# Kernel tuning notes

Hardware: AMD Instinct MI355X
Metric: run time of the kernel (lower is better)

## Reference

```python
import jax, jax.numpy as jnp
import numpy as np

B, T, D, F, E = 2, 2048, 1024, 4096, 8
TOP_K = 2


def setup_inputs() -> dict:
    key = jax.random.key(0)
    k0, k1, k2, k3 = jax.random.split(key, 4)
    x = jax.random.normal(k0, (B, T, D), dtype=jnp.float32)
    Wr = jax.random.normal(k1, (D, E), dtype=jnp.float32) * 0.02   # router (no bias)
    W1 = jax.random.normal(k2, (E, D, F), dtype=jnp.float32) * 0.02
    b1 = jnp.zeros((E, F), dtype=jnp.float32)
    W2 = jax.random.normal(k3, (E, F, D), dtype=jnp.float32) * 0.02
    b2 = jnp.zeros((E, D), dtype=jnp.float32)
    return {"x": x, "Wr": Wr, "W1": W1, "b1": b1, "W2": W2, "b2": b2}


def reference(x, Wr, W1, b1, W2, b2):
    # Router: softmax over experts, top-k select, renormalize selected probs.
    logits = jnp.einsum('btd,de->bte', x, Wr)                      # [B,T,E]
    probs = jax.nn.softmax(logits, axis=-1)
    top_v, top_i = jax.lax.top_k(probs, TOP_K)                     # [B,T,K]
    top_v = top_v / jnp.sum(top_v, axis=-1, keepdims=True)
    # Combine weights: scatter renormalized top-k probs back to expert slots.
    combine = jnp.sum(jax.nn.one_hot(top_i, E, dtype=x.dtype) * top_v[..., None], axis=-2)  # [B,T,E]
    # Expert FFNs (Linear -> exact GELU -> Linear); dropout inactive at eval.
    h = jax.nn.gelu(jnp.einsum('btd,edf->ebtf', x, W1) + b1[:, None, None, :],
                    approximate=False)                              # [E,B,T,F]
    y = jnp.einsum('ebtf,efd->ebtd', h, W2) + b2[:, None, None, :]  # [E,B,T,D]
    # Weighted sum over selected experts (combine is zero for unselected).
    out = jnp.einsum('ebtd,bte->btd', y, combine)
    return out
```

## Files before the change

### kernel.cpp

```cpp
#include <hip/hip_runtime.h>
#include <hip/hip_bf16.h>
#include <math.h>

#define B_  2
#define T_  2048
#define D_  1024
#define F_  4096
#define E_  8
#define NTOK 4096
#define TOPK 2
#define NROW 8192

typedef unsigned short bf16_t;
typedef float f32x4 __attribute__((ext_vector_type(4)));
typedef int   i32x4 __attribute__((ext_vector_type(4)));

#define OFF_CNT   0
#define OFF_BASE  32
#define OFF_TIDX  64
#define OFF_TW    32832
#define OFF_LIST  65600
#define OFF_WGT   196672
#define OFF_H_OLD 327744
#define WS_OLD    (OFF_H_OLD + (size_t)NROW * F_ * 2)
#define OFF_SLOT  327744
#define OFF_XB    (1u << 20)
#define OFF_W1T   (OFF_XB  + (size_t)NTOK * D_ * 2)
#define OFF_W2T   (OFF_W1T + (size_t)E_ * F_ * D_ * 2)
#define OFF_HN    (OFF_W2T + (size_t)E_ * D_ * F_ * 2)
#define OFF_Y     (OFF_HN  + (size_t)NROW * F_ * 2)
#define WS_MFMA   (OFF_Y + (size_t)NROW * D_ * 4)
#define WS_MFMA2  (OFF_Y + 2 * (size_t)NROW * D_ * 4)

__device__ __forceinline__ float gelu_exact(float v) {
    return 0.5f * v * (1.0f + erff(v * 0.70710678118654752440f));
}

__device__ __forceinline__ unsigned short f2bf_rne(float f) {
    union { float f; unsigned int u; } v; v.f = f;
    unsigned int r = (v.u + 0x7fffu + ((v.u >> 16) & 1u)) >> 16;
    return (unsigned short)r;
}

__device__ __forceinline__ float bf2f(unsigned int u) {
    union { unsigned int i; float f; } v; v.i = u << 16; return v.f;
}

__device__ __forceinline__ void gld16(const void* g, void* l) {
    __builtin_amdgcn_global_load_lds(
        (const __attribute__((address_space(1))) unsigned int*)g,
        (__attribute__((address_space(3))) unsigned int*)l, 16, 0, 0);
}

__device__ __forceinline__ void mfma16(const i32x4& a, const i32x4& b, f32x4& c) {
    asm("v_mfma_f32_16x16x32_bf16 %0, %1, %2, %0" : "+v"(c) : "v"(a), "v"(b));
}

__global__ __launch_bounds__(64) void router_kernel(
    const float* __restrict__ x, const float* __restrict__ Wr,
    int* __restrict__ top_idx, float* __restrict__ top_w,
    int* __restrict__ cnt, int* __restrict__ list, float* __restrict__ wgt,
    int* __restrict__ slot, int mode)
{
    const int n = blockIdx.x;
    const int lane = threadIdx.x;
    const float* xr = x + (size_t)n * D_;

    float acc[E_];
#pragma unroll
    for (int e = 0; e < E_; ++e) acc[e] = 0.f;

    for (int d = lane; d < D_; d += 64) {
        const float xv = xr[d];
#pragma unroll
        for (int e = 0; e < E_; ++e)
            acc[e] += xv * Wr[d * E_ + e];
    }
#pragma unroll
    for (int e = 0; e < E_; ++e) {
        float v = acc[e];
#pragma unroll
        for (int off = 32; off > 0; off >>= 1)
            v += __shfl_down(v, off, 64);
        acc[e] = v;
    }
    if (lane == 0) {
        float m = acc[0];
#pragma unroll
        for (int e = 1; e < E_; ++e) m = fmaxf(m, acc[e]);
        float p[E_];
#pragma unroll
        for (int e = 0; e < E_; ++e) p[e] = __expf(acc[e] - m);
        int i0 = 0; float v0 = p[0];
#pragma unroll
        for (int e = 1; e < E_; ++e) if (p[e] > v0) { v0 = p[e]; i0 = e; }
        int i1 = (i0 == 0) ? 1 : 0; float v1 = p[i1];
#pragma unroll
        for (int e = 0; e < E_; ++e) {
            if (e == i0) continue;
            if (p[e] > v1) { v1 = p[e]; i1 = e; }
        }
        const float inv = 1.f / (v0 + v1);
        const float w0 = v0 * inv, w1 = v1 * inv;
        top_idx[n * TOPK + 0] = i0;
        top_idx[n * TOPK + 1] = i1;
        top_w[n * TOPK + 0] = w0;
        top_w[n * TOPK + 1] = w1;
        if (mode & 1) {
            int p0 = atomicAdd(&cnt[i0], 1);
            list[i0 * NTOK + p0] = n;  wgt[i0 * NTOK + p0] = w0;
            int p1 = atomicAdd(&cnt[i1], 1);
            list[i1 * NTOK + p1] = n;  wgt[i1 * NTOK + p1] = w1;
            if (mode & 2) {
                slot[n * TOPK + 0] = (i0 << 16) | p0;
                slot[n * TOPK + 1] = (i1 << 16) | p1;
            }
        }
    }
}

__global__ void prefix_kernel(const int* __restrict__ cnt, int* __restrict__ base)
{
    if (threadIdx.x == 0 && blockIdx.x == 0) {
        int s = 0;
#pragma unroll
        for (int e = 0; e < E_; ++e) { base[e] = s; s += cnt[e]; }
    }
}

__global__ __launch_bounds__(256) void convert_x_kernel(
    const float* __restrict__ x, bf16_t* __restrict__ xb)
{
    const int i = blockIdx.x * 256 + threadIdx.x;
    const float4 v = ((const float4*)x)[i];
    uint2 o;
    o.x = (unsigned int)f2bf_rne(v.x) | ((unsigned int)f2bf_rne(v.y) << 16);
    o.y = (unsigned int)f2bf_rne(v.z) | ((unsigned int)f2bf_rne(v.w) << 16);
    ((uint2*)xb)[i] = o;
}

__global__ __launch_bounds__(256) void transpose_kernel(
    const float* __restrict__ src, bf16_t* __restrict__ dst, int R, int C)
{
    __shared__ float tile[64][65];
    const int z  = blockIdx.z;
    const int r0 = blockIdx.y * 64;
    const int c0 = blockIdx.x * 64;
    const float* s = src + (size_t)z * R * C;
    bf16_t*      d = dst + (size_t)z * R * C;
    const int tx = threadIdx.x & 63;
    const int ty = threadIdx.x >> 6;
#pragma unroll
    for (int i = 0; i < 16; ++i) {
        const int r = i * 4 + ty;
        tile[r][tx] = s[(size_t)(r0 + r) * C + c0 + tx];
    }
    __syncthreads();
    const int rc = (threadIdx.x & 15) * 4;
    const int cc = threadIdx.x >> 4;
#pragma unroll
    for (int i = 0; i < 4; ++i) {
        const int c = i * 16 + cc;
        uint2 o;
        o.x = (unsigned int)f2bf_rne(tile[rc    ][c]) | ((unsigned int)f2bf_rne(tile[rc + 1][c]) << 16);
        o.y = (unsigned int)f2bf_rne(tile[rc + 2][c]) | ((unsigned int)f2bf_rne(tile[rc + 3][c]) << 16);
        *(uint2*)(d + (size_t)(c0 + c) * R + r0 + rc) = o;
    }
}

__global__ __launch_bounds__(256) void mgemm1_kernel(
    const bf16_t* __restrict__ Xb, const bf16_t* __restrict__ W1T,
    const float* __restrict__ b1,
    const int* __restrict__ cnt, const int* __restrict__ base,
    const int* __restrict__ list, bf16_t* __restrict__ H)
{
    __shared__ __align__(16) bf16_t As[2][128 * 32];
    __shared__ __align__(16) bf16_t Bs[2][128 * 32];

    const int e  = blockIdx.z;
    const int ce = cnt[e];
    const int m0 = blockIdx.y * 128;
    if (m0 >= ce) return;
    const int n0 = blockIdx.x * 128;
    const int be = base[e];
    const int tid  = threadIdx.x;
    const int lane = tid & 63, wave = tid >> 6;
    const int wr = wave >> 1, wc = wave & 1;
    const int quad = lane >> 4, l16 = lane & 15;

    const int mA = tid >> 2, cA = tid & 3;
    int r0i = m0 + mA;        if (r0i >= ce) r0i = ce - 1;
    int r1i = m0 + mA + 64;   if (r1i >= ce) r1i = ce - 1;
    const bf16_t* gA0 = Xb + (size_t)list[e * NTOK + r0i] * D_ + cA * 8;
    const bf16_t* gA1 = Xb + (size_t)list[e * NTOK + r1i] * D_ + cA * 8;
    const bf16_t* W1Te = W1T + (size_t)e * F_ * D_;
    const bf16_t* gB0 = W1Te + (size_t)(n0 + mA) * D_ + cA * 8;
    const bf16_t* gB1 = W1Te + (size_t)(n0 + mA + 64) * D_ + cA * 8;

    f32x4 acc[4][4] = {};

#define PREF1(bufi, kk) do { \
        gld16(gA0 + (kk), As[bufi] + wave * 512); \
        gld16(gA1 + (kk), As[bufi] + 2048 + wave * 512); \
        gld16(gB0 + (kk), Bs[bufi] + wave * 512); \
        gld16(gB1 + (kk), Bs[bufi] + 2048 + wave * 512); } while (0)

    PREF1(0, 0);
    int buf = 0;
    for (int k0 = 0; k0 < D_; k0 += 32) {
        __syncthreads();
        if (k0 + 32 < D_) PREF1(buf ^ 1, k0 + 32);
        i32x4 af[4], bfv[4];
#pragma unroll
        for (int i = 0; i < 4; ++i) {
            af[i]  = *(const i32x4*)(As[buf] + (wr * 64 + i * 16 + l16) * 32 + quad * 8);
            bfv[i] = *(const i32x4*)(Bs[buf] + (wc * 64 + i * 16 + l16) * 32 + quad * 8);
        }
#pragma unroll
        for (int i = 0; i < 4; ++i)
#pragma unroll
            for (int j = 0; j < 4; ++j)
                mfma16(af[i], bfv[j], acc[i][j]);
        buf ^= 1;
    }
#undef PREF1
    asm volatile("s_nop 7\n\ts_nop 7");

    const float* b1e = b1 + (size_t)e * F_;
#pragma unroll
    for (int i = 0; i < 4; ++i) {
        const int rl = wr * 64 + i * 16 + quad * 4;
#pragma unroll
        for (int j = 0; j < 4; ++j) {
            const int col = n0 + wc * 64 + j * 16 + l16;
            const float bb = b1e[col];
#pragma unroll
            for (int r = 0; r < 4; ++r) {
                const int p = m0 + rl + r;
                if (p < ce)
                    H[(size_t)(be + p) * F_ + col] = f2bf_rne(gelu_exact(acc[i][j][r] + bb));
            }
        }
    }
}

__global__ __launch_bounds__(256) void mgemm2_kernel(
    const bf16_t* __restrict__ H, const bf16_t* __restrict__ W2T,
    const float* __restrict__ b2,
    const int* __restrict__ cnt, const int* __restrict__ base,
    float* __restrict__ Y)
{
    __shared__ __align__(16) bf16_t As[2][128 * 32];
    __shared__ __align__(16) bf16_t Bs[2][128 * 32];

    const int kslabs = gridDim.z / E_;
    const int e  = blockIdx.z % E_;
    const int s  = blockIdx.z / E_;
    const int ce = cnt[e];
    const int m0 = blockIdx.y * 128;
    if (m0 >= ce) return;
    const int klen  = F_ / kslabs;
    const int kbase = s * klen;
    const int n0 = blockIdx.x * 128;
    const int be = base[e];
    const int tid  = threadIdx.x;
    const int lane = tid & 63, wave = tid >> 6;
    const int wr = wave >> 1, wc = wave & 1;
    const int quad = lane >> 4, l16 = lane & 15;

    const int mA = tid >> 2, cA = tid & 3;
    int r0i = m0 + mA;        if (r0i >= ce) r0i = ce - 1;
    int r1i = m0 + mA + 64;   if (r1i >= ce) r1i = ce - 1;
    const bf16_t* gA0 = H + (size_t)(be + r0i) * F_ + cA * 8 + kbase;
    const bf16_t* gA1 = H + (size_t)(be + r1i) * F_ + cA * 8 + kbase;
    const bf16_t* W2Te = W2T + (size_t)e * D_ * F_;
    const bf16_t* gB0 = W2Te + (size_t)(n0 + mA) * F_ + cA * 8 + kbase;
    const bf16_t* gB1 = W2Te + (size_t)(n0 + mA + 64) * F_ + cA * 8 + kbase;

    f32x4 acc[4][4] = {};

#define PREF2(bufi, kk) do { \
        gld16(gA0 + (kk), As[bufi] + wave * 512); \
        gld16(gA1 + (kk), As[bufi] + 2048 + wave * 512); \
        gld16(gB0 + (kk), Bs[bufi] + wave * 512); \
        gld16(gB1 + (kk), Bs[bufi] + 2048 + wave * 512); } while (0)

    PREF2(0, 0);
    int buf = 0;
    for (int k0 = 0; k0 < klen; k0 += 32) {
        __syncthreads();
        if (k0 + 32 < klen) PREF2(buf ^ 1, k0 + 32);
        i32x4 af[4], bfv[4];
#pragma unroll
        for (int i = 0; i < 4; ++i) {
            af[i]  = *(const i32x4*)(As[buf] + (wr * 64 + i * 16 + l16) * 32 + quad * 8);
            bfv[i] = *(const i32x4*)(Bs[buf] + (wc * 64 + i * 16 + l16) * 32 + quad * 8);
        }
#pragma unroll
        for (int i = 0; i < 4; ++i)
#pragma unroll
            for (int j = 0; j < 4; ++j)
                mfma16(af[i], bfv[j], acc[i][j]);
        buf ^= 1;
    }
#undef PREF2
    asm volatile("s_nop 7\n\ts_nop 7");

    float* Ys = Y + (size_t)s * NROW * D_;
    const float* b2e = b2 + (size_t)e * D_;
#pragma unroll
    for (int i = 0; i < 4; ++i) {
        const int rl = wr * 64 + i * 16 + quad * 4;
#pragma unroll
        for (int j = 0; j < 4; ++j) {
            const int col = n0 + wc * 64 + j * 16 + l16;
            const float bb = (s == 0) ? b2e[col] : 0.f;
#pragma unroll
            for (int r = 0; r < 4; ++r) {
                const int p = m0 + rl + r;
                if (p < ce)
                    Ys[(size_t)(be + p) * D_ + col] = acc[i][j][r] + bb;
            }
        }
    }
}

__global__ __launch_bounds__(256) void combine_kernel(
    const float* __restrict__ Y, const int* __restrict__ slot,
    const float* __restrict__ tw, const int* __restrict__ base,
    float* __restrict__ out, int kslabs)
{
    const int n = blockIdx.x;
    const int t = threadIdx.x;
    const int s0 = slot[n * TOPK + 0], s1 = slot[n * TOPK + 1];
    const float w0 = tw[n * TOPK + 0], w1 = tw[n * TOPK + 1];
    const int r0 = base[s0 >> 16] + (s0 & 0xffff);
    const int r1 = base[s1 >> 16] + (s1 & 0xffff);
    float4 y0 = ((const float4*)(Y + (size_t)r0 * D_))[t];
    float4 y1 = ((const float4*)(Y + (size_t)r1 * D_))[t];
    if (kslabs == 2) {
        const float* Y1 = Y + (size_t)NROW * D_;
        const float4 a = ((const float4*)(Y1 + (size_t)r0 * D_))[t];
        const float4 b = ((const float4*)(Y1 + (size_t)r1 * D_))[t];
        y0.x += a.x; y0.y += a.y; y0.z += a.z; y0.w += a.w;
        y1.x += b.x; y1.y += b.y; y1.z += b.z; y1.w += b.w;
    }
    float4 o;
    o.x = w0 * y0.x + w1 * y1.x;
    o.y = w0 * y0.y + w1 * y1.y;
    o.z = w0 * y0.z + w1 * y1.z;
    o.w = w0 * y0.w + w1 * y1.w;
    ((float4*)(out + (size_t)n * D_))[t] = o;
}

#define BM 128
#define BN 128
#define BK 16

__global__ __launch_bounds__(256) void gemm1_kernel(
    const float* __restrict__ x, const float* __restrict__ W1,
    const float* __restrict__ b1,
    const int* __restrict__ cnt, const int* __restrict__ base,
    const int* __restrict__ list, bf16_t* __restrict__ H)
{
    __shared__ __align__(16) float Xs[BK][BM + 4];
    __shared__ __align__(16) float Ws[BK][BN + 4];

    const int e  = blockIdx.z;
    const int ce = cnt[e];
    const int m0 = blockIdx.y * BM;
    if (m0 >= ce) return;
    const int n0 = blockIdx.x * BN;
    const int be = base[e];
    const int t  = threadIdx.x;
    const int tx = t & 15, ty = t >> 4;

    const int xr_row = t >> 1;
    const int xr_c0  = (t & 1) * 8;
    const int p_x    = m0 + xr_row;
    const float* xrow = (p_x < ce) ? (x + (size_t)list[e * NTOK + p_x] * D_) : nullptr;
    const int wr_kk = t >> 4;
    const int wr_c0 = (t & 15) * 8;
    const float* W1e = W1 + (size_t)e * D_ * F_;

    float acc[8][8];
#pragma unroll
    for (int i = 0; i < 8; ++i)
#pragma unroll
        for (int j = 0; j < 8; ++j) acc[i][j] = 0.f;

    for (int k0 = 0; k0 < D_; k0 += BK) {
        float xv[8];
        if (xrow) {
            const float4 a = *(const float4*)(xrow + k0 + xr_c0);
            const float4 b = *(const float4*)(xrow + k0 + xr_c0 + 4);
            xv[0]=a.x; xv[1]=a.y; xv[2]=a.z; xv[3]=a.w;
            xv[4]=b.x; xv[5]=b.y; xv[6]=b.z; xv[7]=b.w;
        } else {
#pragma unroll
            for (int j = 0; j < 8; ++j) xv[j] = 0.f;
        }
#pragma unroll
        for (int j = 0; j < 8; ++j) Xs[xr_c0 + j][xr_row] = xv[j];
        {
            const float* wr = W1e + (size_t)(k0 + wr_kk) * F_ + (n0 + wr_c0);
            *(float4*)&Ws[wr_kk][wr_c0]     = *(const float4*)(wr);
            *(float4*)&Ws[wr_kk][wr_c0 + 4] = *(const float4*)(wr + 4);
        }
        __syncthreads();
#pragma unroll 4
        for (int kk = 0; kk < BK; ++kk) {
            float a[8], b[8];
            *(float4*)&a[0] = *(const float4*)&Xs[kk][ty * 8];
            *(float4*)&a[4] = *(const float4*)&Xs[kk][ty * 8 + 4];
            *(float4*)&b[0] = *(const float4*)&Ws[kk][tx * 8];
            *(float4*)&b[4] = *(const float4*)&Ws[kk][tx * 8 + 4];
#pragma unroll
            for (int i = 0; i < 8; ++i)
#pragma unroll
                for (int j = 0; j < 8; ++j)
                    acc[i][j] += a[i] * b[j];
        }
        __syncthreads();
    }

    const float* b1e = b1 + (size_t)e * F_;
    float bb[8];
#pragma unroll
    for (int j = 0; j < 8; ++j) bb[j] = b1e[n0 + tx * 8 + j];
#pragma unroll
    for (int i = 0; i < 8; ++i) {
        const int p = m0 + ty * 8 + i;
        if (p >= ce) continue;
        unsigned int pk[4];
#pragma unroll
        for (int jj = 0; jj < 4; ++jj) {
            const float g0 = gelu_exact(acc[i][2 * jj]     + bb[2 * jj]);
            const float g1 = gelu_exact(acc[i][2 * jj + 1] + bb[2 * jj + 1]);
            pk[jj] = (unsigned int)f2bf_rne(g0) | ((unsigned int)f2bf_rne(g1) << 16);
        }
        uint4 v; v.x = pk[0]; v.y = pk[1]; v.z = pk[2]; v.w = pk[3];
        *(uint4*)(H + (size_t)(be + p) * F_ + n0 + tx * 8) = v;
    }
}

__global__ __launch_bounds__(256) void gemm2_kernel(
    const bf16_t* __restrict__ H, const float* __restrict__ W2,
    const float* __restrict__ b2,
    const int* __restrict__ cnt, const int* __restrict__ base,
    const int* __restrict__ list, const float* __restrict__ wgt,
    float* __restrict__ out)
{
    __shared__ __align__(16) float Hs[BK][BM + 4];
    __shared__ __align__(16) float Ws[BK][BN + 4];

    const int e  = blockIdx.z;
    const int ce = cnt[e];
    const int m0 = blockIdx.y * BM;
    if (m0 >= ce) return;
    const int n0 = blockIdx.x * BN;
    const int be = base[e];
    const int t  = threadIdx.x;
    const int tx = t & 15, ty = t >> 4;

    const int hr_row = t >> 1;
    const int hr_c0  = (t & 1) * 8;
    const int p_h    = m0 + hr_row;
    const bf16_t* hrow = (p_h < ce) ? (H + (size_t)(be + p_h) * F_) : nullptr;
    const int wr_kk = t >> 4;
    const int wr_c0 = (t & 15) * 8;
    const float* W2e = W2 + (size_t)e * F_ * D_;

    float acc[8][8];
#pragma unroll
    for (int i = 0; i < 8; ++i)
#pragma unroll
        for (int j = 0; j < 8; ++j) acc[i][j] = 0.f;

    for (int k0 = 0; k0 < F_; k0 += BK) {
        float hv[8];
        if (hrow) {
            const uint4 u = *(const uint4*)(hrow + k0 + hr_c0);
            hv[0] = bf2f(u.x & 0xffffu); hv[1] = bf2f(u.x >> 16);
            hv[2] = bf2f(u.y & 0xffffu); hv[3] = bf2f(u.y >> 16);
            hv[4] = bf2f(u.z & 0xffffu); hv[5] = bf2f(u.z >> 16);
            hv[6] = bf2f(u.w & 0xffffu); hv[7] = bf2f(u.w >> 16);
        } else {
#pragma unroll
            for (int j = 0; j < 8; ++j) hv[j] = 0.f;
        }
#pragma unroll
        for (int j = 0; j < 8; ++j) Hs[hr_c0 + j][hr_row] = hv[j];
        {
            const float* wr = W2e + (size_t)(k0 + wr_kk) * D_ + (n0 + wr_c0);
            *(float4*)&Ws[wr_kk][wr_c0]     = *(const float4*)(wr);
            *(float4*)&Ws[wr_kk][wr_c0 + 4] = *(const float4*)(wr + 4);
        }
        __syncthreads();
#pragma unroll 4
        for (int kk = 0; kk < BK; ++kk) {
            float a[8], b[8];
            *(float4*)&a[0] = *(const float4*)&Hs[kk][ty * 8];
            *(float4*)&a[4] = *(const float4*)&Hs[kk][ty * 8 + 4];
            *(float4*)&b[0] = *(const float4*)&Ws[kk][tx * 8];
            *(float4*)&b[4] = *(const float4*)&Ws[kk][tx * 8 + 4];
#pragma unroll
            for (int i = 0; i < 8; ++i)
#pragma unroll
                for (int j = 0; j < 8; ++j)
                    acc[i][j] += a[i] * b[j];
        }
        __syncthreads();
    }

    const float* b2e = b2 + (size_t)e * D_;
    float bb[8];
#pragma unroll
    for (int j = 0; j < 8; ++j) bb[j] = b2e[n0 + tx * 8 + j];
#pragma unroll
    for (int i = 0; i < 8; ++i) {
        const int p = m0 + ty * 8 + i;
        if (p >= ce) continue;
        const int   n = list[e * NTOK + p];
        const float w = wgt[e * NTOK + p];
        float* op = out + (size_t)n * D_ + n0 + tx * 8;
#pragma unroll
        for (int j = 0; j < 8; ++j)
            atomicAdd(&op[j], w * (acc[i][j] + bb[j]));
    }
}

__global__ __launch_bounds__(256) void fallback_expert_kernel(
    const float* __restrict__ x,
    const float* __restrict__ W1, const float* __restrict__ b1,
    const float* __restrict__ W2, const float* __restrict__ b2,
    const int* __restrict__ top_idx, const float* __restrict__ top_w,
    float* __restrict__ out)
{
    __shared__ float x_lds[D_];
    __shared__ float h_lds[F_];

    const int n = blockIdx.x;
    const int t = threadIdx.x;

    ((float4*)x_lds)[t] = ((const float4*)(x + (size_t)n * D_))[t];
    __syncthreads();

    const int d0 = t * 4;
    float acc_out[4] = {0.f, 0.f, 0.f, 0.f};

    for (int k = 0; k < TOPK; ++k) {
        const int   e = top_idx[n * TOPK + k];
        const float w = top_w[n * TOPK + k];
        const float* W1e = W1 + (size_t)e * D_ * F_;
        const float* b1e = b1 + (size_t)e * F_;
#pragma unroll
        for (int tile = 0; tile < 2; ++tile) {
            const int base_f = tile * 2048 + t * 8;
            float a[8];
#pragma unroll
            for (int j = 0; j < 8; ++j) a[j] = b1e[base_f + j];
            const float4* wp = (const float4*)(W1e + base_f);
            for (int d = 0; d < D_; ++d) {
                const float4 w0 = wp[(size_t)d * (F_ / 4)];
                const float4 w1 = wp[(size_t)d * (F_ / 4) + 1];
                const float xv = x_lds[d];
                a[0] += xv * w0.x; a[1] += xv * w0.y;
                a[2] += xv * w0.z; a[3] += xv * w0.w;
                a[4] += xv * w1.x; a[5] += xv * w1.y;
                a[6] += xv * w1.z; a[7] += xv * w1.w;
            }
#pragma unroll
            for (int j = 0; j < 8; ++j)
                h_lds[base_f + j] = gelu_exact(a[j]);
        }
        __syncthreads();

        const float* W2e = W2 + (size_t)e * F_ * D_;
        const float* b2e = b2 + (size_t)e * D_;
        float y[4];
#pragma unroll
        for (int j = 0; j < 4; ++j) y[j] = b2e[d0 + j];
        const float4* wp2 = (const float4*)(W2e + d0);
        for (int f = 0; f < F_; ++f) {
            const float4 wv = wp2[(size_t)f * (D_ / 4)];
            const float hv = h_lds[f];
            y[0] += hv * wv.x; y[1] += hv * wv.y;
            y[2] += hv * wv.z; y[3] += hv * wv.w;
        }
#pragma unroll
        for (int j = 0; j < 4; ++j) acc_out[j] += w * y[j];
        __syncthreads();
    }

    float4 o; o.x = acc_out[0]; o.y = acc_out[1]; o.z = acc_out[2]; o.w = acc_out[3];
    *(float4*)(out + (size_t)n * D_ + d0) = o;
}

extern "C" void kernel_launch(void* const* d_in, const int* in_sizes, int n_in,
                              void* d_out, int out_size, void* d_ws, size_t ws_size,
                              hipStream_t stream) {
    const float* x  = (const float*)d_in[0];
    const float* Wr = (const float*)d_in[1];
    const float* W1 = (const float*)d_in[2];
    const float* b1 = (const float*)d_in[3];
    const float* W2 = (const float*)d_in[4];
    const float* b2 = (const float*)d_in[5];
    float* out = (float*)d_out;

    char* ws = (char*)d_ws;
    int*    cnt   = (int*)(ws + OFF_CNT);
    int*    basep = (int*)(ws + OFF_BASE);
    int*    tidx  = (int*)(ws + OFF_TIDX);
    float*  tw    = (float*)(ws + OFF_TW);
    int*    list  = (int*)(ws + OFF_LIST);
    float*  wgt   = (float*)(ws + OFF_WGT);

    if (ws_size >= WS_MFMA) {
        const int kslabs = (ws_size >= WS_MFMA2) ? 2 : 1;
        int*    slot = (int*)(ws + OFF_SLOT);
        bf16_t* Xb   = (bf16_t*)(ws + OFF_XB);
        bf16_t* W1T  = (bf16_t*)(ws + OFF_W1T);
        bf16_t* W2T  = (bf16_t*)(ws + OFF_W2T);
        bf16_t* H    = (bf16_t*)(ws + OFF_HN);
        float*  Y    = (float*)(ws + OFF_Y);

        hipMemsetAsync(cnt, 0, E_ * sizeof(int), stream);
        router_kernel<<<NTOK, 64, 0, stream>>>(x, Wr, tidx, tw, cnt, list, wgt, slot, 3);
        prefix_kernel<<<1, 64, 0, stream>>>(cnt, basep);
        convert_x_kernel<<<NTOK * D_ / 4 / 256, 256, 0, stream>>>(x, Xb);
        transpose_kernel<<<dim3(F_ / 64, D_ / 64, E_), 256, 0, stream>>>(W1, W1T, D_, F_);
        transpose_kernel<<<dim3(D_ / 64, F_ / 64, E_), 256, 0, stream>>>(W2, W2T, F_, D_);
        mgemm1_kernel<<<dim3(F_ / 128, NTOK / 128, E_), 256, 0, stream>>>(
            Xb, W1T, b1, cnt, basep, list, H);
        mgemm2_kernel<<<dim3(D_ / 128, NTOK / 128, E_ * kslabs), 256, 0, stream>>>(
            H, W2T, b2, cnt, basep, Y);
        combine_kernel<<<NTOK, 256, 0, stream>>>(Y, slot, tw, basep, out, kslabs);
    } else if (ws_size >= WS_OLD) {
        bf16_t* H = (bf16_t*)(ws + OFF_H_OLD);
        hipMemsetAsync(cnt, 0, E_ * sizeof(int), stream);
        router_kernel<<<NTOK, 64, 0, stream>>>(x, Wr, tidx, tw, cnt, list, wgt, nullptr, 1);
        prefix_kernel<<<1, 64, 0, stream>>>(cnt, basep);
        hipMemsetAsync(out, 0, (size_t)NTOK * D_ * sizeof(float), stream);
        gemm1_kernel<<<dim3(F_ / BN, NTOK / BM, E_), 256, 0, stream>>>(
            x, W1, b1, cnt, basep, list, H);
        gemm2_kernel<<<dim3(D_ / BN, NTOK / BM, E_), 256, 0, stream>>>(
            H, W2, b2, cnt, basep, list, wgt, out);
    } else {
        router_kernel<<<NTOK, 64, 0, stream>>>(x, Wr, tidx, tw, cnt, list, wgt, nullptr, 0);
        fallback_expert_kernel<<<NTOK, 256, 0, stream>>>(
            x, W1, b1, W2, b2, tidx, tw, out);
    }
}
```

Measured before the change: 711.3 us.

## Merge expert GEMMs into 256x256-tile triple-buffered MFMA kernel with swizzled LDS

Replaces the two 128x128-tile, double-buffered expert GEMM kernels with one templated kernel. It uses 256x256 tiles, 512 threads (8 waves), a three-stage LDS ring with explicit vmcnt waits and raw barriers, an XOR-swizzled LDS layout to cut bank conflicts, and raised wave priority around the MFMA block. The weight transpose kernel also now loads float4 vectors. Larger tiles raise data reuse per byte loaded, but they increase register and LDS pressure (96KB shared) and waste more work on the padded tail of each expert's ragged row count.

```diff
diff --git a/kernel.cpp b/kernel.cpp
--- a/kernel.cpp
+++ b/kernel.cpp
@@ -148,12 +148,15 @@
     const int c0 = blockIdx.x * 64;
     const float* s = src + (size_t)z * R * C;
     bf16_t*      d = dst + (size_t)z * R * C;
-    const int tx = threadIdx.x & 63;
-    const int ty = threadIdx.x >> 6;
-#pragma unroll
-    for (int i = 0; i < 16; ++i) {
-        const int r = i * 4 + ty;
-        tile[r][tx] = s[(size_t)(r0 + r) * C + c0 + tx];
+#pragma unroll
+    for (int i = 0; i < 4; ++i) {
+        const int r  = i * 16 + (threadIdx.x >> 4);
+        const int c4 = (threadIdx.x & 15) * 4;
+        const float4 v = *(const float4*)(s + (size_t)(r0 + r) * C + c0 + c4);
+        tile[r][c4]     = v.x;
+        tile[r][c4 + 1] = v.y;
+        tile[r][c4 + 2] = v.z;
+        tile[r][c4 + 3] = v.w;
     }
     __syncthreads();
     const int rc = (threadIdx.x & 15) * 4;
@@ -168,158 +171,141 @@
     }
 }
 
-__global__ __launch_bounds__(256) void mgemm1_kernel(
-    const bf16_t* __restrict__ Xb, const bf16_t* __restrict__ W1T,
-    const float* __restrict__ b1,
+template<int G>
+__global__ __launch_bounds__(512, 2) void mg8_kernel(
+    const bf16_t* __restrict__ Amat, const bf16_t* __restrict__ Bmat,
+    const float* __restrict__ bias,
     const int* __restrict__ cnt, const int* __restrict__ base,
-    const int* __restrict__ list, bf16_t* __restrict__ H)
-{
-    __shared__ __align__(16) bf16_t As[2][128 * 32];
-    __shared__ __align__(16) bf16_t Bs[2][128 * 32];
-
-    const int e  = blockIdx.z;
+    const int* __restrict__ list,
+    bf16_t* __restrict__ Hout, float* __restrict__ Yout)
+{
+    __shared__ __align__(16) bf16_t sm[3 * 16384];
+
+    const int e  = (G == 1) ? blockIdx.z : (blockIdx.z % E_);
     const int ce = cnt[e];
-    const int m0 = blockIdx.y * 128;
+    const int m0 = blockIdx.y * 256;
     if (m0 >= ce) return;
-    const int n0 = blockIdx.x * 128;
+    const int n0 = blockIdx.x * 256;
     const int be = base[e];
+
+    const int Kfull = (G == 1) ? D_ : F_;
+    int klen, kbase, slab;
+    if (G == 1) { klen = D_; kbase = 0; slab = 0; }
+    else {
+        const int kslabs = gridDim.z / E_;
+        slab  = blockIdx.z / E_;
+        klen  = F_ / kslabs;
+        kbase = slab * klen;
+    }
+    const int nk = klen / 32;
+
     const int tid  = threadIdx.x;
     const int lane = tid & 63, wave = tid >> 6;
-    const int wr = wave >> 1, wc = wave & 1;
-    const int quad = lane >> 4, l16 = lane & 15;
-
-    const int mA = tid >> 2, cA = tid & 3;
-    int r0i = m0 + mA;        if (r0i >= ce) r0i = ce - 1;
-    int r1i = m0 + mA + 64;   if (r1i >= ce) r1i = ce - 1;
-    const bf16_t* gA0 = Xb + (size_t)list[e * NTOK + r0i] * D_ + cA * 8;
-    const bf16_t* gA1 = Xb + (size_t)list[e * NTOK + r1i] * D_ + cA * 8;
-    const bf16_t* W1Te = W1T + (size_t)e * F_ * D_;
-    const bf16_t* gB0 = W1Te + (size_t)(n0 + mA) * D_ + cA * 8;
-    const bf16_t* gB1 = W1Te + (size_t)(n0 + mA + 64) * D_ + cA * 8;
-
-    f32x4 acc[4][4] = {};
-
-#define PREF1(bufi, kk) do { \
-        gld16(gA0 + (kk), As[bufi] + wave * 512); \
-        gld16(gA1 + (kk), As[bufi] + 2048 + wave * 512); \
-        gld16(gB0 + (kk), Bs[bufi] + wave * 512); \
-        gld16(gB1 + (kk), Bs[bufi] + 2048 + wave * 512); } while (0)
-
-    PREF1(0, 0);
-    int buf = 0;
-    for (int k0 = 0; k0 < D_; k0 += 32) {
-        __syncthreads();
-        if (k0 + 32 < D_) PREF1(buf ^ 1, k0 + 32);
-        i32x4 af[4], bfv[4];
-#pragma unroll
-        for (int i = 0; i < 4; ++i) {
-            af[i]  = *(const i32x4*)(As[buf] + (wr * 64 + i * 16 + l16) * 32 + quad * 8);
-            bfv[i] = *(const i32x4*)(Bs[buf] + (wc * 64 + i * 16 + l16) * 32 + quad * 8);
-        }
-#pragma unroll
-        for (int i = 0; i < 4; ++i)
-#pragma unroll
-            for (int j = 0; j < 4; ++j)
-                mfma16(af[i], bfv[j], acc[i][j]);
-        buf ^= 1;
-    }
-#undef PREF1
+    const int l16 = lane & 15, quad = lane >> 4;
+    const int wm = wave >> 2, wn = wave & 3;
+
+    const int srow = wave * 16 + (lane >> 2);
+    const int sgc  = (lane & 3) ^ ((srow >> 1) & 3);
+    int rA0 = m0 + srow;        if (rA0 >= ce) rA0 = ce - 1;
+    int rA1 = m0 + srow + 128;  if (rA1 >= ce) rA1 = ce - 1;
+    const bf16_t *gA0, *gA1;
+    if (G == 1) {
+        gA0 = Amat + (size_t)list[e * NTOK + rA0] * D_ + sgc * 8;
+        gA1 = Amat + (size_t)list[e * NTOK + rA1] * D_ + sgc * 8;
+    } else {
+        gA0 = Amat + (size_t)(be + rA0) * F_ + kbase + sgc * 8;
+        gA1 = Amat + (size_t)(be + rA1) * F_ + kbase + sgc * 8;
+    }
+    const bf16_t* Be  = Bmat + (size_t)e * F_ * D_;
+    const bf16_t* gB0 = Be + (size_t)(n0 + srow) * Kfull + kbase + sgc * 8;
+    const bf16_t* gB1 = Be + (size_t)(n0 + srow + 128) * Kfull + kbase + sgc * 8;
+
+#define STG(bb, kk) do { \
+        bf16_t* la = sm + (bb) * 16384 + wave * 512; \
+        bf16_t* lb = la + 8192; \
+        gld16(gA0 + (kk), la); \
+        gld16(gA1 + (kk), la + 4096); \
+        gld16(gB0 + (kk), lb); \
+        gld16(gB1 + (kk), lb + 4096); } while (0)
+
+    const int swz  = (quad ^ ((l16 >> 1) & 3)) * 8;
+    const int aoff = (wm * 128 + l16) * 32 + swz;
+    const int boff = 8192 + (wn * 64 + l16) * 32 + swz;
+
+    f32x4 acc[8][4] = {};
+
+    STG(0, 0);
+    STG(1, 32);
+    asm volatile("s_waitcnt vmcnt(4)" ::: "memory");
+    __builtin_amdgcn_s_barrier();
+    __builtin_amdgcn_sched_barrier(0);
+
+    int rb = 0;
+    for (int t = 0; t < nk; ++t) {
+        if (t + 2 < nk) {
+            int wb = rb + 2; if (wb >= 3) wb -= 3;
+            STG(wb, (t + 2) * 32);
+        }
+        const bf16_t* bp = sm + rb * 16384;
+        i32x4 af[8], bv[4];
+#pragma unroll
+        for (int m = 0; m < 8; ++m)
+            af[m] = *(const i32x4*)(bp + aoff + m * 512);
+#pragma unroll
+        for (int n = 0; n < 4; ++n)
+            bv[n] = *(const i32x4*)(bp + boff + n * 512);
+        __builtin_amdgcn_s_setprio(1);
+#pragma unroll
+        for (int m = 0; m < 8; ++m)
+#pragma unroll
+            for (int n = 0; n < 4; ++n)
+                mfma16(af[m], bv[n], acc[m][n]);
+        __builtin_amdgcn_s_setprio(0);
+        if (t + 1 < nk) {
+            if (t + 2 < nk) asm volatile("s_waitcnt vmcnt(4)" ::: "memory");
+            else            asm volatile("s_waitcnt vmcnt(0)" ::: "memory");
+            __builtin_amdgcn_s_barrier();
+            __builtin_amdgcn_sched_barrier(0);
+        }
+        rb = (rb == 2) ? 0 : rb + 1;
+    }
+#undef STG
     asm volatile("s_nop 7\n\ts_nop 7");
 
-    const float* b1e = b1 + (size_t)e * F_;
-#pragma unroll
-    for (int i = 0; i < 4; ++i) {
-        const int rl = wr * 64 + i * 16 + quad * 4;
-#pragma unroll
-        for (int j = 0; j < 4; ++j) {
-            const int col = n0 + wc * 64 + j * 16 + l16;
+    if (G == 1) {
+        const float* b1e = bias + (size_t)e * F_;
+#pragma unroll
+        for (int n = 0; n < 4; ++n) {
+            const int col = n0 + wn * 64 + n * 16 + l16;
             const float bb = b1e[col];
 #pragma unroll
-            for (int r = 0; r < 4; ++r) {
-                const int p = m0 + rl + r;
-                if (p < ce)
-                    H[(size_t)(be + p) * F_ + col] = f2bf_rne(gelu_exact(acc[i][j][r] + bb));
+            for (int m = 0; m < 8; ++m) {
+                const int pr = m0 + wm * 128 + m * 16 + quad * 4;
+#pragma unroll
+                for (int r = 0; r < 4; ++r) {
+                    const int p = pr + r;
+                    if (p < ce)
+                        Hout[(size_t)(be + p) * F_ + col] =
+                            f2bf_rne(gelu_exact(acc[m][n][r] + bb));
+                }
             }
         }
-    }
-}
-
-__global__ __launch_bounds__(256) void mgemm2_kernel(
-    const bf16_t* __restrict__ H, const bf16_t* __restrict__ W2T,
-    const float* __restrict__ b2,
-    const int* __restrict__ cnt, const int* __restrict__ base,
-    float* __restrict__ Y)
-{
-    __shared__ __align__(16) bf16_t As[2][128 * 32];
-    __shared__ __align__(16) bf16_t Bs[2][128 * 32];
-
-    const int kslabs = gridDim.z / E_;
-    const int e  = blockIdx.z % E_;
-    const int s  = blockIdx.z / E_;
-    const int ce = cnt[e];
-    const int m0 = blockIdx.y * 128;
-    if (m0 >= ce) return;
-    const int klen  = F_ / kslabs;
-    const int kbase = s * klen;
-    const int n0 = blockIdx.x * 128;
-    const int be = base[e];
-    const int tid  = threadIdx.x;
-    const int lane = tid & 63, wave = tid >> 6;
-    const int wr = wave >> 1, wc = wave & 1;
-    const int quad = lane >> 4, l16 = lane & 15;
-
-    const int mA = tid >> 2, cA = tid & 3;
-    int r0i = m0 + mA;        if (r0i >= ce) r0i = ce - 1;
-    int r1i = m0 + mA + 64;   if (r1i >= ce) r1i = ce - 1;
-    const bf16_t* gA0 = H + (size_t)(be + r0i) * F_ + cA * 8 + kbase;
-    const bf16_t* gA1 = H + (size_t)(be + r1i) * F_ + cA * 8 + kbase;
-    const bf16_t* W2Te = W2T + (size_t)e * D_ * F_;
-    const bf16_t* gB0 = W2Te + (size_t)(n0 + mA) * F_ + cA * 8 + kbase;
-    const bf16_t* gB1 = W2Te + (size_t)(n0 + mA + 64) * F_ + cA * 8 + kbase;
-
-    f32x4 acc[4][4] = {};
-
-#define PREF2(bufi, kk) do { \
-        gld16(gA0 + (kk), As[bufi] + wave * 512); \
-        gld16(gA1 + (kk), As[bufi] + 2048 + wave * 512); \
-        gld16(gB0 + (kk), Bs[bufi] + wave * 512); \
-        gld16(gB1 + (kk), Bs[bufi] + 2048 + wave * 512); } while (0)
-
-    PREF2(0, 0);
-    int buf = 0;
-    for (int k0 = 0; k0 < klen; k0 += 32) {
-        __syncthreads();
-        if (k0 + 32 < klen) PREF2(buf ^ 1, k0 + 32);
-        i32x4 af[4], bfv[4];
-#pragma unroll
-        for (int i = 0; i < 4; ++i) {
-            af[i]  = *(const i32x4*)(As[buf] + (wr * 64 + i * 16 + l16) * 32 + quad * 8);
-            bfv[i] = *(const i32x4*)(Bs[buf] + (wc * 64 + i * 16 + l16) * 32 + quad * 8);
-        }
-#pragma unroll
-        for (int i = 0; i < 4; ++i)
-#pragma unroll
-            for (int j = 0; j < 4; ++j)
-                mfma16(af[i], bfv[j], acc[i][j]);
-        buf ^= 1;
-    }
-#undef PREF2
-    asm volatile("s_nop 7\n\ts_nop 7");
-
-    float* Ys = Y + (size_t)s * NROW * D_;
-    const float* b2e = b2 + (size_t)e * D_;
-#pragma unroll
-    for (int i = 0; i < 4; ++i) {
-        const int rl = wr * 64 + i * 16 + quad * 4;
-#pragma unroll
-        for (int j = 0; j < 4; ++j) {
-            const int col = n0 + wc * 64 + j * 16 + l16;
-            const float bb = (s == 0) ? b2e[col] : 0.f;
-#pragma unroll
-            for (int r = 0; r < 4; ++r) {
-                const int p = m0 + rl + r;
-                if (p < ce)
-                    Ys[(size_t)(be + p) * D_ + col] = acc[i][j][r] + bb;
+    } else {
+        float* Ys = Yout + (size_t)slab * NROW * D_;
+        const float* b2e = bias + (size_t)e * D_;
+#pragma unroll
+        for (int n = 0; n < 4; ++n) {
+            const int col = n0 + wn * 64 + n * 16 + l16;
+            const float bb = (slab == 0) ? b2e[col] : 0.f;
+#pragma unroll
+            for (int m = 0; m < 8; ++m) {
+                const int pr = m0 + wm * 128 + m * 16 + quad * 4;
+#pragma unroll
+                for (int r = 0; r < 4; ++r) {
+                    const int p = pr + r;
+                    if (p < ce)
+                        Ys[(size_t)(be + p) * D_ + col] = acc[m][n][r] + bb;
+                }
             }
         }
     }
@@ -631,10 +617,10 @@
         convert_x_kernel<<<NTOK * D_ / 4 / 256, 256, 0, stream>>>(x, Xb);
         transpose_kernel<<<dim3(F_ / 64, D_ / 64, E_), 256, 0, stream>>>(W1, W1T, D_, F_);
         transpose_kernel<<<dim3(D_ / 64, F_ / 64, E_), 256, 0, stream>>>(W2, W2T, F_, D_);
-        mgemm1_kernel<<<dim3(F_ / 128, NTOK / 128, E_), 256, 0, stream>>>(
-            Xb, W1T, b1, cnt, basep, list, H);
-        mgemm2_kernel<<<dim3(D_ / 128, NTOK / 128, E_ * kslabs), 256, 0, stream>>>(
-            H, W2T, b2, cnt, basep, Y);
+        mg8_kernel<1><<<dim3(F_ / 256, NTOK / 256, E_), 512, 0, stream>>>(
+            Xb, W1T, b1, cnt, basep, list, H, nullptr);
+        mg8_kernel<2><<<dim3(D_ / 256, NTOK / 256, E_ * kslabs), 512, 0, stream>>>(
+            H, W2T, b2, cnt, basep, nullptr, nullptr, Y);
         combine_kernel<<<NTOK, 256, 0, stream>>>(Y, slot, tw, basep, out, kslabs);
     } else if (ws_size >= WS_OLD) {
         bf16_t* H = (bf16_t*)(ws + OFF_H_OLD);
```

New measurement: 736.7 us. 1.04x slower.
